# Optimization experiments

Measured on AMD Instinct MI355X. Metric: run time of the kernel, lower is better.

The kernel has to match this reference:

```python
import jax, jax.numpy as jnp
import numpy as np

ETA = 0.01   # Hebbian learning rate of the plasticity rule
LR = 1.0     # CircuitModel.lr


def setup_inputs() -> dict:
    key = jax.random.key(0)
    k1, k2, k3 = jax.random.split(key, 3)
    B, T, NI, NO, NOBS = 64, 256, 512, 512, 128
    X = jax.random.normal(k1, (B, T, NI), dtype=jnp.float32)
    W_init = jax.random.normal(k2, (B, NO, NI), dtype=jnp.float32) * 0.1
    observed_idx = jnp.sort(jax.random.randint(k3, (NOBS,), 0, NO))
    return {"X": X, "W_init": W_init, "observed_idx": observed_idx}


def reference(X, W_init, observed_idx):
    # X: [B,T,NI], W_init: [B,NO,NI], observed_idx: [NOBS] int
    NO = W_init.shape[1]
    mask = jnp.zeros((NO,), X.dtype).at[observed_idx].set(1.0)  # [NO]

    def step(W, x_t):
        # x_t: [B,NI]
        pre = jnp.einsum('boi,bi->bo', W, x_t)          # [B,NO]
        y = jax.nn.sigmoid(pre)
        m = y[:, observed_idx]                           # [B,NOBS] recorded before masking
        y_sparse = y * mask                              # zero unobserved outputs
        W = W * mask[None, :, None]                      # zero unobserved rows of W
        dW = ETA * (y_sparse[:, :, None] * x_t[:, None, :])  # Hebbian outer product
        return W + LR * dW, m

    _, m_traj = jax.lax.scan(step, W_init, jnp.swapaxes(X, 0, 1))  # [T,B,NOBS]
    return jnp.swapaxes(m_traj, 0, 1)  # [B,T,NOBS]
```

## Files before the change

kernel.cpp:

```cpp
#include <hip/hip_runtime.h>

#define NB   64
#define NT   256
#define NI   512
#define NO   512
#define NOBS 128
#define ETA  0.01f

typedef __attribute__((ext_vector_type(8))) short bf16x8;
typedef __attribute__((ext_vector_type(4))) float f32x4;

#define X4_COUNT  (NB*NT*NI/4)
#define WG4_COUNT (NB*NOBS*NI/4)
#define K0_TOTAL  (X4_COUNT + WG4_COUNT)

__device__ __forceinline__ unsigned short f2bf(float f) {
    unsigned int u = __float_as_uint(f);
    return (unsigned short)((u + 0x7fffu + ((u >> 16) & 1u)) >> 16);
}

__global__ __launch_bounds__(256)
void k0_convert(const float* __restrict__ X, const float* __restrict__ Wi,
                const int* __restrict__ obs,
                unsigned short* __restrict__ Xb, unsigned short* __restrict__ Wg)
{
    int idx = blockIdx.x * 256 + threadIdx.x;
    const int stride = gridDim.x * 256;
    for (; idx < K0_TOTAL; idx += stride) {
        float4 v; ushort4* dst;
        if (idx < X4_COUNT) {
            v = ((const float4*)X)[idx];
            dst = (ushort4*)Xb + idx;
        } else {
            int g = idx - X4_COUNT;
            int row = g >> 7, pos = g & 127;
            int b = row >> 7, j = row & 127;
            v = ((const float4*)(Wi + ((size_t)b * NO + obs[j]) * NI))[pos];
            dst = (ushort4*)Wg + ((size_t)row * 128 + pos);
        }
        *dst = make_ushort4(f2bf(v.x), f2bf(v.y), f2bf(v.z), f2bf(v.w));
    }
}

__global__ __launch_bounds__(256)
void k1_gemm(const unsigned short* __restrict__ Xb,
             const unsigned short* __restrict__ Wg,
             float* __restrict__ Gd, unsigned short* __restrict__ Gh,
             float* __restrict__ P0)
{
    __shared__ unsigned short As[128 * 64];
    __shared__ unsigned short Bs[128 * 64];

    const int tid  = threadIdx.x;
    const int lane = tid & 63;
    const int wv   = tid >> 6;
    const int l16  = lane & 15;
    const int quad = lane >> 4;

    const int b   = blockIdx.x & 63;
    const int sub = blockIdx.x >> 6;

    const unsigned short* xbB = Xb + (size_t)b * NT * NI;
    const unsigned short *aRows, *bRows;
    int bm = 0, bn = 0;
    if (sub < 3) {
        bm = (sub >= 1) ? 1 : 0;
        bn = (sub == 2) ? 1 : 0;
        aRows = xbB + (size_t)bm * 128 * NI;
        bRows = xbB + (size_t)bn * 128 * NI;
    } else {
        const int pb = sub - 3;
        bm = pb;
        aRows = xbB + (size_t)pb * 128 * NI;
        bRows = Wg + (size_t)b * NOBS * NI;
    }

    const int wm = (wv >> 1) * 64;
    const int wn = (wv & 1) * 64;

    f32x4 acc[4][4] = {};

    for (int kb = 0; kb < NI / 64; ++kb) {
        __syncthreads();
#pragma unroll
        for (int it = 0; it < 4; ++it) {
            const int s = it * 256 + tid;
            const int m = s >> 3, c = s & 7;
            const int slot = m * 64 + ((c ^ (m & 7)) * 8);
            const size_t goff = (size_t)m * NI + kb * 64 + c * 8;
            *(bf16x8*)&As[slot] = *(const bf16x8*)(aRows + goff);
            *(bf16x8*)&Bs[slot] = *(const bf16x8*)(bRows + goff);
        }
        __syncthreads();
#pragma unroll
        for (int ks = 0; ks < 2; ++ks) {
            const int q = ks * 4 + quad;
            bf16x8 af[4], bfr[4];
#pragma unroll
            for (int mt = 0; mt < 4; ++mt) {
                const int m = wm + mt * 16 + l16;
                af[mt] = *(const bf16x8*)&As[m * 64 + ((q ^ (m & 7)) * 8)];
            }
#pragma unroll
            for (int nt = 0; nt < 4; ++nt) {
                const int n = wn + nt * 16 + l16;
                bfr[nt] = *(const bf16x8*)&Bs[n * 64 + ((q ^ (n & 7)) * 8)];
            }
#pragma unroll
            for (int mt = 0; mt < 4; ++mt)
#pragma unroll
                for (int nt = 0; nt < 4; ++nt)
                    acc[mt][nt] = __builtin_amdgcn_mfma_f32_16x16x32_bf16(
                        af[mt], bfr[nt], acc[mt][nt], 0, 0, 0);
        }
    }

    if (sub < 3) {
        unsigned short* GhB = Gh + ((size_t)b << 16);
        float* GdB = Gd + ((size_t)b << 12);
#pragma unroll
        for (int mt = 0; mt < 4; ++mt)
#pragma unroll
            for (int nt = 0; nt < 4; ++nt) {
                const int gcol = bn * 128 + wn + nt * 16 + l16;
#pragma unroll
                for (int r = 0; r < 4; ++r) {
                    const int grow = bm * 128 + wm + mt * 16 + quad * 4 + r;
                    const float v = ETA * acc[mt][nt][r];
                    GhB[(size_t)grow * 256 + gcol] = f2bf(v);
                    if ((grow >> 4) == (gcol >> 4))
                        GdB[((grow >> 4) << 8) + ((grow & 15) << 4) + (gcol & 15)] = v;
                }
            }
    } else {
        float* Pb = P0 + (size_t)b * NT * NOBS + (size_t)bm * 128 * NOBS;
#pragma unroll
        for (int mt = 0; mt < 4; ++mt)
#pragma unroll
            for (int nt = 0; nt < 4; ++nt)
#pragma unroll
                for (int r = 0; r < 4; ++r)
                    Pb[(size_t)(wm + mt * 16 + quad * 4 + r) * NOBS
                       + wn + nt * 16 + l16] = acc[mt][nt][r];
    }
}


#define LDROW(Q0, Q1, Q2, Q3, U1)                                          \
    {                                                                      \
        if ((U1) <= 14) {                                                  \
            if ((U1) <= 2)  Q0 = *(const f32x4*)(gdc + (U1) * 16);         \
            if ((U1) <= 6)  Q1 = *(const f32x4*)(gdc + (U1) * 16 + 4);     \
            if ((U1) <= 10) Q2 = *(const f32x4*)(gdc + (U1) * 16 + 8);     \
            Q3 = *(const f32x4*)(gdc + (U1) * 16 + 12);                    \
        }                                                                  \
    }

#define GV(Q0, Q1, Q2, Q3, V)                                              \
    ((V) < 4 ? (Q0)[(V) & 3] : (V) < 8 ? (Q1)[(V) & 3]                     \
             : (V) < 12 ? (Q2)[(V) & 3] : (Q3)[(V) & 3])

#define SCAN_STEP(U, C0, C1, C2, C3, N0, N1, N2, N3)                       \
    {                                                                      \
        LDROW(N0, N1, N2, N3, (U) + 2)                                     \
        const float y = __builtin_amdgcn_rcpf(1.f + __expf(-p[(U)]));      \
        ob[obOff + (size_t)((U) * NOBS)] = y;                              \
        _Pragma("unroll")                                                  \
        for (int v = (U) + 1; v < 16; ++v)                                 \
            p[v] = fmaf(y, GV(C0, C1, C2, C3, v), p[v]);                   \
        if ((U) & 1)                                                       \
            ybf2[cp * 128 + ((U) >> 1) * 16 + j] =                         \
                (unsigned)f2bf(eprev) | ((unsigned)f2bf(y) << 16);         \
        else                                                               \
            eprev = y;                                                     \
    }

__global__ __launch_bounds__(512, 4)
void k2_scan(const float* __restrict__ Gd, const unsigned short* __restrict__ Gh,
             const float* __restrict__ P0, float* __restrict__ out)
{
    __shared__ float gdiag[16 * 16 * 16];
    __shared__ float preS[16 * 17];
    __shared__ unsigned int ybf2[2 * 8 * 16];

    const int tid  = threadIdx.x;
    const int lane = tid & 63;
    const int l16  = lane & 15;
    const int quad = lane >> 4;
    const int w    = __builtin_amdgcn_readfirstlane(tid >> 6);

    const int b  = blockIdx.x & 63;
    const int jg = blockIdx.x >> 6;

    const float* Pb = P0 + (size_t)b * NT * NOBS + jg * 16;
    const unsigned short* GhB = Gh + ((size_t)b << 16);
    float* ob = out + (size_t)b * NT * NOBS + jg * 16;

    {
        const f32x4* gs = (const f32x4*)(Gd + ((size_t)b << 12));
        ((f32x4*)gdiag)[tid]       = gs[tid];
        ((f32x4*)gdiag)[512 + tid] = gs[512 + tid];
    }

    f32x4 acc[2];
#pragma unroll
    for (int s2 = 0; s2 < 2; ++s2)
#pragma unroll
        for (int r = 0; r < 4; ++r)
            acc[s2][r] = Pb[(size_t)(w * 32 + s2 * 16 + quad * 4 + r) * NOBS + l16];

    const int T0 = 2 * w, T1 = 2 * w + 1;

    union AB { bf16x8 v; unsigned int d[4]; };
    AB Acur0, Acur1, Anext0, Anext1;
#pragma unroll
    for (int p2 = 0; p2 < 4; ++p2) {
        Acur0.d[p2] = 0; Acur1.d[p2] = 0; Anext0.d[p2] = 0; Anext1.d[p2] = 0;
    }
    if (quad < 2) {
        if (T0 > 0)
            Acur0.v = *(const bf16x8*)(GhB + (size_t)(T0 * 16 + l16) * 256 + quad * 8);
        Acur1.v = *(const bf16x8*)(GhB + (size_t)(T1 * 16 + l16) * 256 + quad * 8);
    }

    auto scan_chunk = [&](const int c, const f32x4 a) {
#pragma unroll
        for (int r = 0; r < 4; ++r)
            preS[(quad * 4 + r) * 17 + l16] = a[r];
        asm volatile("s_waitcnt lgkmcnt(0)" ::: "memory");
        __builtin_amdgcn_s_setprio(1);
        if (lane < 16) {
            const int j = lane;
            const int cp = c & 1;
            const float* gdc = gdiag + (c << 8);
            const size_t obOff = (size_t)(c << 4) * NOBS + j;
            float p[16];
#pragma unroll
            for (int u = 0; u < 16; ++u) p[u] = preS[u * 17 + j];
            f32x4 Aq0, Aq1, Aq2, Aq3, Bq0, Bq1, Bq2, Bq3, Cq0, Cq1, Cq2, Cq3;
            LDROW(Aq0, Aq1, Aq2, Aq3, 0)
            LDROW(Bq0, Bq1, Bq2, Bq3, 1)
            float eprev = 0.f;
            SCAN_STEP(0,  Aq0, Aq1, Aq2, Aq3, Cq0, Cq1, Cq2, Cq3)
            SCAN_STEP(1,  Bq0, Bq1, Bq2, Bq3, Aq0, Aq1, Aq2, Aq3)
            SCAN_STEP(2,  Cq0, Cq1, Cq2, Cq3, Bq0, Bq1, Bq2, Bq3)
            SCAN_STEP(3,  Aq0, Aq1, Aq2, Aq3, Cq0, Cq1, Cq2, Cq3)
            SCAN_STEP(4,  Bq0, Bq1, Bq2, Bq3, Aq0, Aq1, Aq2, Aq3)
            SCAN_STEP(5,  Cq0, Cq1, Cq2, Cq3, Bq0, Bq1, Bq2, Bq3)
            SCAN_STEP(6,  Aq0, Aq1, Aq2, Aq3, Cq0, Cq1, Cq2, Cq3)
            SCAN_STEP(7,  Bq0, Bq1, Bq2, Bq3, Aq0, Aq1, Aq2, Aq3)
            SCAN_STEP(8,  Cq0, Cq1, Cq2, Cq3, Bq0, Bq1, Bq2, Bq3)
            SCAN_STEP(9,  Aq0, Aq1, Aq2, Aq3, Cq0, Cq1, Cq2, Cq3)
            SCAN_STEP(10, Bq0, Bq1, Bq2, Bq3, Aq0, Aq1, Aq2, Aq3)
            SCAN_STEP(11, Cq0, Cq1, Cq2, Cq3, Bq0, Bq1, Bq2, Bq3)
            SCAN_STEP(12, Aq0, Aq1, Aq2, Aq3, Cq0, Cq1, Cq2, Cq3)
            SCAN_STEP(13, Bq0, Bq1, Bq2, Bq3, Aq0, Aq1, Aq2, Aq3)
            SCAN_STEP(14, Cq0, Cq1, Cq2, Cq3, Bq0, Bq1, Bq2, Bq3)
            SCAN_STEP(15, Aq0, Aq1, Aq2, Aq3, Cq0, Cq1, Cq2, Cq3)
        }
        __builtin_amdgcn_s_setprio(0);
    };

    if (w == 0)
        scan_chunk(0, acc[0]);
    __syncthreads();

#pragma unroll 1
    for (int c = 0; c < 15; ++c) {
        if (T1 > c) {
            AB B;
#pragma unroll
            for (int p2 = 0; p2 < 4; ++p2) B.d[p2] = 0;
            if (quad < 2) {
#pragma unroll
                for (int p2 = 0; p2 < 4; ++p2)
                    B.d[p2] = ybf2[(c & 1) * 128 + (quad * 4 + p2) * 16 + l16];
            }
#pragma unroll
            for (int p2 = 0; p2 < 4; ++p2) { Anext0.d[p2] = 0; Anext1.d[p2] = 0; }
            if (quad < 2) {
                if (T0 > c + 1)
                    Anext0.v = *(const bf16x8*)(GhB + (size_t)(T0 * 16 + l16) * 256
                                                + (c + 1) * 16 + quad * 8);
                if (T1 > c + 1)
                    Anext1.v = *(const bf16x8*)(GhB + (size_t)(T1 * 16 + l16) * 256
                                                + (c + 1) * 16 + quad * 8);
            }
            if (T0 > c)
                acc[0] = __builtin_amdgcn_mfma_f32_16x16x32_bf16(
                    Acur0.v, B.v, acc[0], 0, 0, 0);
            acc[1] = __builtin_amdgcn_mfma_f32_16x16x32_bf16(
                Acur1.v, B.v, acc[1], 0, 0, 0);
            if (w == ((c + 1) >> 1)) {
                if ((c + 1) & 1) scan_chunk(c + 1, acc[1]);
                else             scan_chunk(c + 1, acc[0]);
            }
            Acur0 = Anext0;
            Acur1 = Anext1;
        }
        __syncthreads();
    }
}

extern "C" void kernel_launch(void* const* d_in, const int* in_sizes, int n_in,
                              void* d_out, int out_size, void* d_ws, size_t ws_size,
                              hipStream_t stream)
{
    const float* X   = (const float*)d_in[0];
    const float* Wi  = (const float*)d_in[1];
    const int*   obs = (const int*)d_in[2];
    float*       out = (float*)d_out;

    float*          Gd = (float*)d_ws;
    float*          P0 = (float*)((char*)d_ws + (1u << 20));
    unsigned short* Gh = (unsigned short*)((char*)d_ws + (9u << 20));
    unsigned short* Xb = (unsigned short*)((char*)d_ws + (17u << 20));
    unsigned short* Wg = (unsigned short*)((char*)d_ws + (33u << 20));

    hipLaunchKernelGGL(k0_convert, dim3(3072), dim3(256), 0, stream,
                       X, Wi, obs, Xb, Wg);
    hipLaunchKernelGGL(k1_gemm, dim3(NB * 5), dim3(256), 0, stream,
                       Xb, Wg, Gd, Gh, P0);
    hipLaunchKernelGGL(k2_scan, dim3(NB * 8), dim3(512), 0, stream,
                       Gd, Gh, P0, out);
}
```

Baseline: 155.3 us.

## Fuse fp32-to-bf16 conversion and observed-row gather into GEMM tile loads

Removes the separate conversion kernel that wrote bf16 copies of X and the gathered W rows to workspace. The GEMM now reads fp32 X and W directly, gathering observed rows through an index table held in shared memory. It converts to bf16 in registers with the packed v_cvt_pk_bf16_f32 instruction before the LDS store. This saves one launch and a full write-then-read pass over the bf16 intermediates, but the GEMM now loads twice the bytes per tile, and X is re-read by several blocks in fp32.

```diff
diff --git a/kernel.cpp b/kernel.cpp
--- a/kernel.cpp
+++ b/kernel.cpp
@@ -10,46 +10,26 @@
 typedef __attribute__((ext_vector_type(8))) short bf16x8;
 typedef __attribute__((ext_vector_type(4))) float f32x4;
 
-#define X4_COUNT  (NB*NT*NI/4)
-#define WG4_COUNT (NB*NOBS*NI/4)
-#define K0_TOTAL  (X4_COUNT + WG4_COUNT)
-
 __device__ __forceinline__ unsigned short f2bf(float f) {
     unsigned int u = __float_as_uint(f);
     return (unsigned short)((u + 0x7fffu + ((u >> 16) & 1u)) >> 16);
 }
 
+__device__ __forceinline__ unsigned cvtpk(float lo, float hi) {
+    unsigned r;
+    asm("v_cvt_pk_bf16_f32 %0, %1, %2" : "=v"(r) : "v"(lo), "v"(hi));
+    return r;
+}
+
 __global__ __launch_bounds__(256)
-void k0_convert(const float* __restrict__ X, const float* __restrict__ Wi,
-                const int* __restrict__ obs,
-                unsigned short* __restrict__ Xb, unsigned short* __restrict__ Wg)
-{
-    int idx = blockIdx.x * 256 + threadIdx.x;
-    const int stride = gridDim.x * 256;
-    for (; idx < K0_TOTAL; idx += stride) {
-        float4 v; ushort4* dst;
-        if (idx < X4_COUNT) {
-            v = ((const float4*)X)[idx];
-            dst = (ushort4*)Xb + idx;
-        } else {
-            int g = idx - X4_COUNT;
-            int row = g >> 7, pos = g & 127;
-            int b = row >> 7, j = row & 127;
-            v = ((const float4*)(Wi + ((size_t)b * NO + obs[j]) * NI))[pos];
-            dst = (ushort4*)Wg + ((size_t)row * 128 + pos);
-        }
-        *dst = make_ushort4(f2bf(v.x), f2bf(v.y), f2bf(v.z), f2bf(v.w));
-    }
-}
-
-__global__ __launch_bounds__(256)
-void k1_gemm(const unsigned short* __restrict__ Xb,
-             const unsigned short* __restrict__ Wg,
+void k1_gemm(const float* __restrict__ Xf, const float* __restrict__ Wf,
+             const int* __restrict__ obs,
              float* __restrict__ Gd, unsigned short* __restrict__ Gh,
              float* __restrict__ P0)
 {
     __shared__ unsigned short As[128 * 64];
     __shared__ unsigned short Bs[128 * 64];
+    __shared__ int obsS[128];
 
     const int tid  = threadIdx.x;
     const int lane = tid & 63;
@@ -60,19 +40,30 @@
     const int b   = blockIdx.x & 63;
     const int sub = blockIdx.x >> 6;
 
-    const unsigned short* xbB = Xb + (size_t)b * NT * NI;
-    const unsigned short *aRows, *bRows;
+    if (tid < 128) obsS[tid] = obs[tid];
+    __syncthreads();
+
     int bm = 0, bn = 0;
     if (sub < 3) {
         bm = (sub >= 1) ? 1 : 0;
         bn = (sub == 2) ? 1 : 0;
-        aRows = xbB + (size_t)bm * 128 * NI;
-        bRows = xbB + (size_t)bn * 128 * NI;
     } else {
-        const int pb = sub - 3;
-        bm = pb;
-        aRows = xbB + (size_t)pb * 128 * NI;
-        bRows = Wg + (size_t)b * NOBS * NI;
+        bm = sub - 3;
+    }
+
+    const int mrow = tid >> 3;
+    const int ccol = tid & 7;
+    const float* aP[4];
+    const float* bP[4];
+    int slotv[4];
+#pragma unroll
+    for (int it = 0; it < 4; ++it) {
+        const int m = it * 32 + mrow;
+        slotv[it] = m * 64 + ((ccol ^ (m & 7)) * 8);
+        aP[it] = Xf + ((size_t)b * NT + bm * 128 + m) * NI + ccol * 8;
+        bP[it] = (sub < 3)
+                   ? Xf + ((size_t)b * NT + bn * 128 + m) * NI + ccol * 8
+                   : Wf + ((size_t)b * NO + obsS[m]) * NI + ccol * 8;
     }
 
     const int wm = (wv >> 1) * 64;
@@ -84,12 +75,19 @@
         __syncthreads();
 #pragma unroll
         for (int it = 0; it < 4; ++it) {
-            const int s = it * 256 + tid;
-            const int m = s >> 3, c = s & 7;
-            const int slot = m * 64 + ((c ^ (m & 7)) * 8);
-            const size_t goff = (size_t)m * NI + kb * 64 + c * 8;
-            *(bf16x8*)&As[slot] = *(const bf16x8*)(aRows + goff);
-            *(bf16x8*)&Bs[slot] = *(const bf16x8*)(bRows + goff);
+            const float4 a0 = *(const float4*)(aP[it]);
+            const float4 a1 = *(const float4*)(aP[it] + 4);
+            const float4 b0 = *(const float4*)(bP[it]);
+            const float4 b1 = *(const float4*)(bP[it] + 4);
+            uint4 ap, bp;
+            ap.x = cvtpk(a0.x, a0.y); ap.y = cvtpk(a0.z, a0.w);
+            ap.z = cvtpk(a1.x, a1.y); ap.w = cvtpk(a1.z, a1.w);
+            bp.x = cvtpk(b0.x, b0.y); bp.y = cvtpk(b0.z, b0.w);
+            bp.z = cvtpk(b1.x, b1.y); bp.w = cvtpk(b1.z, b1.w);
+            *(uint4*)&As[slotv[it]] = ap;
+            *(uint4*)&Bs[slotv[it]] = bp;
+            aP[it] += 64;
+            bP[it] += 64;
         }
         __syncthreads();
 #pragma unroll
@@ -314,13 +312,9 @@
     float*          Gd = (float*)d_ws;
     float*          P0 = (float*)((char*)d_ws + (1u << 20));
     unsigned short* Gh = (unsigned short*)((char*)d_ws + (9u << 20));
-    unsigned short* Xb = (unsigned short*)((char*)d_ws + (17u << 20));
-    unsigned short* Wg = (unsigned short*)((char*)d_ws + (33u << 20));
-
-    hipLaunchKernelGGL(k0_convert, dim3(3072), dim3(256), 0, stream,
-                       X, Wi, obs, Xb, Wg);
+
     hipLaunchKernelGGL(k1_gemm, dim3(NB * 5), dim3(256), 0, stream,
-                       Xb, Wg, Gd, Gh, P0);
+                       X, Wi, obs, Gd, Gh, P0);
     hipLaunchKernelGGL(k2_scan, dim3(NB * 8), dim3(512), 0, stream,
                        Gd, Gh, P0, out);
 }
```

Result: faster. 147.7 us (median of 2 runs) (-4.9%).
